# Performance work log

Hardware: AMD Instinct MI355X
Metric: run time of the kernel (lower is better)

## Reference

```python
import jax, jax.numpy as jnp
import numpy as np

N = 50000
E = 800000
IN_CH = 64
HID = 32
HEADS = 8
OUT_CH = 32
NEG_SLOPE = 0.2  # PyG GATConv default leaky_relu slope


def gat_conv(x, src, dst, W, a_src, a_dst, bias, heads, out_ch, concat, n_nodes):
    # x: [N, F_in]; W: [F_in, heads*out_ch]; a_*: [heads, out_ch]; bias: [heads*out_ch] or [out_ch]
    h = (x @ W).reshape(n_nodes, heads, out_ch)            # [N, H, C]
    alpha_s = jnp.sum(h * a_src, axis=-1)                  # [N, H]
    alpha_d = jnp.sum(h * a_dst, axis=-1)                  # [N, H]
    e = jax.nn.leaky_relu(alpha_s[src] + alpha_d[dst], NEG_SLOPE)  # [E, H]
    # segment softmax over destination node
    m = jax.ops.segment_max(e, dst, num_segments=n_nodes)  # [N, H]
    ex = jnp.exp(e - m[dst])                               # [E, H]
    denom = jax.ops.segment_sum(ex, dst, num_segments=n_nodes)  # [N, H]
    alpha = ex / (denom[dst] + 1e-16)                      # [E, H]
    out = jax.ops.segment_sum(alpha[:, :, None] * h[src], dst, num_segments=n_nodes)  # [N, H, C]
    out = out.reshape(n_nodes, heads * out_ch) if concat else out.mean(axis=1)
    return out + bias


def setup_inputs() -> dict:
    key = jax.random.key(0)
    ks = jax.random.split(key, 12)
    x = jax.random.normal(ks[0], (N, IN_CH), dtype=jnp.float32)
    edge_index = jax.random.randint(ks[1], (2, E), 0, N, dtype=jnp.int32)
    s1 = 1.0 / np.sqrt(IN_CH)
    s2 = 1.0 / np.sqrt(HEADS * HID)
    W1 = jax.random.uniform(ks[2], (IN_CH, HEADS * HID), jnp.float32, -s1, s1)
    a_src1 = jax.random.uniform(ks[3], (HEADS, HID), jnp.float32, -s2, s2)
    a_dst1 = jax.random.uniform(ks[4], (HEADS, HID), jnp.float32, -s2, s2)
    b1 = jnp.zeros((HEADS * HID,), jnp.float32)
    W2 = jax.random.uniform(ks[5], (HEADS * HID, OUT_CH), jnp.float32, -s2, s2)
    a_src2 = jax.random.uniform(ks[6], (1, OUT_CH), jnp.float32, -s2, s2)
    a_dst2 = jax.random.uniform(ks[7], (1, OUT_CH), jnp.float32, -s2, s2)
    b2 = jnp.zeros((OUT_CH,), jnp.float32)
    return {"x": x, "edge_index": edge_index, "W1": W1, "a_src1": a_src1,
            "a_dst1": a_dst1, "b1": b1, "W2": W2, "a_src2": a_src2,
            "a_dst2": a_dst2, "b2": b2}


def reference(x, edge_index, W1, a_src1, a_dst1, b1, W2, a_src2, a_dst2, b2):
    # add self-loops (PyG GATConv default)
    loops = jnp.arange(N, dtype=edge_index.dtype)
    src = jnp.concatenate([edge_index[0], loops])
    dst = jnp.concatenate([edge_index[1], loops])
    h = gat_conv(x, src, dst, W1, a_src1, a_dst1, b1, HEADS, HID, True, N)
    h = jax.nn.relu(h)  # dropout inactive in eval
    out = gat_conv(h, src, dst, W2, a_src2, a_dst2, b2, 1, OUT_CH, False, N)
    return jax.nn.log_softmax(out, axis=1)
```

## Files before the change

### kernel.cpp

```cpp
#include <hip/hip_runtime.h>
#include <math.h>
#include <stdint.h>

#define NN 50000
#define NE 800000
#define INC 64
#define HEADS 8
#define F1 256
#define OC 32
#define NEGS 0.2f
#define CSTR 64
#define G1B 1564

typedef unsigned short ushort_t;
typedef float floatx2 __attribute__((ext_vector_type(2)));

__device__ __forceinline__ ushort_t f2bf(float f) {
    uint32_t u = __builtin_bit_cast(uint32_t, f);
    uint32_t r = (u + 0x7fffu + ((u >> 16) & 1u)) >> 16;
    return (ushort_t)r;
}
__device__ __forceinline__ float bflo(uint32_t p) { return __builtin_bit_cast(float, p << 16); }
__device__ __forceinline__ float bfhi(uint32_t p) { return __builtin_bit_cast(float, p & 0xffff0000u); }
__device__ __forceinline__ float bf2f(ushort_t v) { return __builtin_bit_cast(float, (uint32_t)v << 16); }

#if __has_builtin(__builtin_amdgcn_cvt_pk_fp8_f32) && __has_builtin(__builtin_amdgcn_cvt_pk_f32_fp8)
#define HW_FP8 1
#endif

__device__ __forceinline__ uint32_t f2e4m3_sw(float x) {
    float a = fabsf(x);
    uint32_t s = (__builtin_bit_cast(uint32_t, x) >> 31) << 7;
    if (a < 0.015625f) {
        uint32_t m = (uint32_t)rintf(a * 512.0f);
        return s | m;
    }
    if (a >= 448.f) return s | 0x7e;
    uint32_t u = __builtin_bit_cast(uint32_t, a);
    int E = (int)((u >> 23) & 255) - 127;
    float scale = __builtin_bit_cast(float, (uint32_t)(3 - E + 127) << 23);
    uint32_t q = (uint32_t)rintf(a * scale);
    if (q == 16) { E += 1; q = 8; }
    return s | ((uint32_t)(E + 7) << 3) | (q - 8);
}
__device__ __forceinline__ float e4m3f_sw(uint32_t b) {
    uint32_t e = (b >> 3) & 15, m = b & 7;
    float v;
    if (e) v = __builtin_bit_cast(float, ((e + 120u) << 23) | (m << 20));
    else   v = (float)m * 0.001953125f;
    return (b & 0x80u) ? -v : v;
}

__device__ __forceinline__ uint32_t pack4_fp8(float a, float b, float c, float d) {
#ifdef HW_FP8
    int v = __builtin_amdgcn_cvt_pk_fp8_f32(a, b, 0, false);
    v = __builtin_amdgcn_cvt_pk_fp8_f32(c, d, v, true);
    return (uint32_t)v;
#else
    return f2e4m3_sw(a) | (f2e4m3_sw(b) << 8) | (f2e4m3_sw(c) << 16) | (f2e4m3_sw(d) << 24);
#endif
}
__device__ __forceinline__ void unpack4_fp8(uint32_t r, float& f0, float& f1, float& f2, float& f3) {
#ifdef HW_FP8
    floatx2 lo = __builtin_amdgcn_cvt_pk_f32_fp8((int)r, false);
    floatx2 hi = __builtin_amdgcn_cvt_pk_f32_fp8((int)r, true);
    f0 = lo[0]; f1 = lo[1]; f2 = hi[0]; f3 = hi[1];
#else
    f0 = e4m3f_sw(r & 255); f1 = e4m3f_sw((r >> 8) & 255);
    f2 = e4m3f_sw((r >> 16) & 255); f3 = e4m3f_sw(r >> 24);
#endif
}

__global__ __launch_bounds__(256) void k_gemm1(
    const float* __restrict__ x, const float* __restrict__ W1,
    const float* __restrict__ a_s, const float* __restrict__ a_d,
    uint8_t* __restrict__ h1, float* __restrict__ alpha_s, float* __restrict__ alpha_d,
    const int* __restrict__ ei, int* __restrict__ pos, ushort_t* __restrict__ csr_src)
{
    __shared__ float Wl[INC][128];
    __shared__ float xt[INC][64];
    int t = threadIdx.x;
    int gb = blockIdx.x;
    int ntile = gb >> 1;
    int hc = gb & 1;
    int nb = ntile * 64;

    {
        const float* Wsrc = W1 + hc * 128;
        for (int i = t; i < 2048; i += 256) {
            int k = i >> 5, c4 = (i & 31) << 2;
            *(float4*)&Wl[k][c4] = *(const float4*)(Wsrc + k * F1 + c4);
        }
    }
    {
        int n = t >> 2;
        int kq = (t & 3) << 4;
        int gn = nb + n;
        if (gn < NN) {
            const float* xr = x + (size_t)gn * INC + kq;
#pragma unroll
            for (int j = 0; j < 16; j += 4) {
                float4 v = *(const float4*)(xr + j);
                xt[kq + j + 0][n] = v.x; xt[kq + j + 1][n] = v.y;
                xt[kq + j + 2][n] = v.z; xt[kq + j + 3][n] = v.w;
            }
        } else {
#pragma unroll
            for (int j = 0; j < 16; ++j) xt[kq + j][n] = 0.f;
        }
    }
    __syncthreads();

    int lane = t & 63, w = t >> 6;
    int ng = lane >> 5;
    int c0 = (lane & 31) << 2;
    int nbase = (w << 4) + (ng << 3);

    float acc[8][4];
#pragma unroll
    for (int i = 0; i < 8; i++) { acc[i][0] = acc[i][1] = acc[i][2] = acc[i][3] = 0.f; }

#pragma unroll 2
    for (int k = 0; k < INC; ++k) {
        float4 wv = *(const float4*)&Wl[k][c0];
        const float4* xs = (const float4*)&xt[k][nbase];
        float4 xa = xs[0], xb = xs[1];
        float xq[8];
        xq[0] = xa.x; xq[1] = xa.y; xq[2] = xa.z; xq[3] = xa.w;
        xq[4] = xb.x; xq[5] = xb.y; xq[6] = xb.z; xq[7] = xb.w;
#pragma unroll
        for (int ns = 0; ns < 8; ++ns) {
            float xvv = xq[ns];
            acc[ns][0] = fmaf(xvv, wv.x, acc[ns][0]);
            acc[ns][1] = fmaf(xvv, wv.y, acc[ns][1]);
            acc[ns][2] = fmaf(xvv, wv.z, acc[ns][2]);
            acc[ns][3] = fmaf(xvv, wv.w, acc[ns][3]);
        }
    }

    int cglob = hc * 128 + c0;
    float4 av = *(const float4*)(a_s + cglob);
    float4 dv = *(const float4*)(a_d + cglob);
    int head = hc * 4 + ((lane & 31) >> 3);
#pragma unroll
    for (int ns = 0; ns < 8; ++ns) {
        int n = nb + nbase + ns;
        if (n < NN) {
            uint32_t pk = pack4_fp8(acc[ns][0], acc[ns][1], acc[ns][2], acc[ns][3]);
            *(uint32_t*)(h1 + (size_t)n * F1 + cglob) = pk;
            float ps = acc[ns][0] * av.x + acc[ns][1] * av.y + acc[ns][2] * av.z + acc[ns][3] * av.w;
            float pd = acc[ns][0] * dv.x + acc[ns][1] * dv.y + acc[ns][2] * dv.z + acc[ns][3] * dv.w;
            ps += __shfl_xor(ps, 1); ps += __shfl_xor(ps, 2); ps += __shfl_xor(ps, 4);
            pd += __shfl_xor(pd, 1); pd += __shfl_xor(pd, 2); pd += __shfl_xor(pd, 4);
            if ((lane & 7) == 0) {
                alpha_s[n * HEADS + head] = ps;
                alpha_d[n * HEADS + head] = pd;
            }
        }
    }

    {
        int e0 = gb * 512 + t;
#pragma unroll
        for (int q = 0; q < 2; ++q) {
            int e = e0 + q * 256;
            if (e < NE) {
                int s = ei[e];
                int d = ei[NE + e];
                int r = atomicAdd(&pos[d], 1);
                if (r < CSTR) csr_src[d * CSTR + r] = (ushort_t)s;
            }
        }
    }
}

__global__ __launch_bounds__(256) void k_gather1(
    const uint8_t* __restrict__ h1,
    const float* __restrict__ alpha_s, const float* __restrict__ alpha_d,
    const int* __restrict__ pos, const ushort_t* __restrict__ csr_src,
    const float* __restrict__ b1, ushort_t* __restrict__ h1rb)
{
    int wid = (blockIdx.x * blockDim.x + threadIdx.x) >> 6;
    if (wid >= NN) return;
    int lane = threadIdx.x & 63;
    int d = wid;
    int deg = pos[d]; deg = (deg < CSTR) ? deg : CSTR;
    const ushort_t* lst = csr_src + d * CSTR;
    int hh = lane >> 3;
    float ad = alpha_d[d * HEADS + hh];
    int cb = lane << 2;
    const uint8_t* hbase = h1 + cb;

    float4 A0 = {0.f, 0.f, 0.f, 0.f}, A1 = {0.f, 0.f, 0.f, 0.f};
    float dn0 = 0.f, dn1 = 0.f;

    {
        float e = alpha_s[d * HEADS + hh] + ad;
        uint32_t r = *(const uint32_t*)(hbase + (size_t)d * F1);
        e = (e > 0.f) ? e : NEGS * e;
        float w = __expf(e);
        float f0, f1, f2, f3;
        unpack4_fp8(r, f0, f1, f2, f3);
        dn0 += w;
        A0.x = fmaf(w, f0, A0.x); A0.y = fmaf(w, f1, A0.y);
        A0.z = fmaf(w, f2, A0.z); A0.w = fmaf(w, f3, A0.w);
    }

    int i = 0;
    for (; i + 8 <= deg; i += 8) {
        uint4 p4 = *(const uint4*)(lst + i);
        int s[8];
        s[0] = p4.x & 0xffff; s[1] = p4.x >> 16;
        s[2] = p4.y & 0xffff; s[3] = p4.y >> 16;
        s[4] = p4.z & 0xffff; s[5] = p4.z >> 16;
        s[6] = p4.w & 0xffff; s[7] = p4.w >> 16;
        float e[8];
#pragma unroll
        for (int j = 0; j < 8; ++j) e[j] = alpha_s[s[j] * HEADS + hh] + ad;
        uint32_t r[8];
#pragma unroll
        for (int j = 0; j < 8; ++j) r[j] = *(const uint32_t*)(hbase + (size_t)s[j] * F1);
#pragma unroll
        for (int j = 0; j < 8; ++j) {
            float tt = e[j];
            tt = (tt > 0.f) ? tt : NEGS * tt;
            float w = __expf(tt);
            float f0, f1, f2, f3;
            unpack4_fp8(r[j], f0, f1, f2, f3);
            if (j & 1) {
                dn1 += w;
                A1.x = fmaf(w, f0, A1.x); A1.y = fmaf(w, f1, A1.y);
                A1.z = fmaf(w, f2, A1.z); A1.w = fmaf(w, f3, A1.w);
            } else {
                dn0 += w;
                A0.x = fmaf(w, f0, A0.x); A0.y = fmaf(w, f1, A0.y);
                A0.z = fmaf(w, f2, A0.z); A0.w = fmaf(w, f3, A0.w);
            }
        }
    }
    for (; i + 4 <= deg; i += 4) {
        uint2 p2 = *(const uint2*)(lst + i);
        int s0 = p2.x & 0xffff, s1 = p2.x >> 16, s2 = p2.y & 0xffff, s3 = p2.y >> 16;
        float e0 = alpha_s[s0 * HEADS + hh] + ad;
        float e1 = alpha_s[s1 * HEADS + hh] + ad;
        float e2 = alpha_s[s2 * HEADS + hh] + ad;
        float e3 = alpha_s[s3 * HEADS + hh] + ad;
        uint32_t r0 = *(const uint32_t*)(hbase + (size_t)s0 * F1);
        uint32_t r1 = *(const uint32_t*)(hbase + (size_t)s1 * F1);
        uint32_t r2 = *(const uint32_t*)(hbase + (size_t)s2 * F1);
        uint32_t r3 = *(const uint32_t*)(hbase + (size_t)s3 * F1);
        e0 = (e0 > 0.f) ? e0 : NEGS * e0;
        e1 = (e1 > 0.f) ? e1 : NEGS * e1;
        e2 = (e2 > 0.f) ? e2 : NEGS * e2;
        e3 = (e3 > 0.f) ? e3 : NEGS * e3;
        float w0 = __expf(e0), w1 = __expf(e1), w2 = __expf(e2), w3 = __expf(e3);
        float f0, f1, f2, f3;
        dn0 += w0; dn1 += w1; dn0 += w2; dn1 += w3;
        unpack4_fp8(r0, f0, f1, f2, f3);
        A0.x = fmaf(w0, f0, A0.x); A0.y = fmaf(w0, f1, A0.y);
        A0.z = fmaf(w0, f2, A0.z); A0.w = fmaf(w0, f3, A0.w);
        unpack4_fp8(r1, f0, f1, f2, f3);
        A1.x = fmaf(w1, f0, A1.x); A1.y = fmaf(w1, f1, A1.y);
        A1.z = fmaf(w1, f2, A1.z); A1.w = fmaf(w1, f3, A1.w);
        unpack4_fp8(r2, f0, f1, f2, f3);
        A0.x = fmaf(w2, f0, A0.x); A0.y = fmaf(w2, f1, A0.y);
        A0.z = fmaf(w2, f2, A0.z); A0.w = fmaf(w2, f3, A0.w);
        unpack4_fp8(r3, f0, f1, f2, f3);
        A1.x = fmaf(w3, f0, A1.x); A1.y = fmaf(w3, f1, A1.y);
        A1.z = fmaf(w3, f2, A1.z); A1.w = fmaf(w3, f3, A1.w);
    }
    for (; i < deg; ++i) {
        int s = lst[i];
        float e = alpha_s[s * HEADS + hh] + ad;
        uint32_t r = *(const uint32_t*)(hbase + (size_t)s * F1);
        e = (e > 0.f) ? e : NEGS * e;
        float w = __expf(e);
        float f0, f1, f2, f3;
        unpack4_fp8(r, f0, f1, f2, f3);
        dn0 += w;
        A0.x = fmaf(w, f0, A0.x); A0.y = fmaf(w, f1, A0.y);
        A0.z = fmaf(w, f2, A0.z); A0.w = fmaf(w, f3, A0.w);
    }
    float inv = 1.0f / (dn0 + dn1 + 1e-16f);
    float4 bv = *(const float4*)(b1 + cb);
    ushort4 o;
    o.x = f2bf(fmaxf(fmaf(A0.x + A1.x, inv, bv.x), 0.f));
    o.y = f2bf(fmaxf(fmaf(A0.y + A1.y, inv, bv.y), 0.f));
    o.z = f2bf(fmaxf(fmaf(A0.z + A1.z, inv, bv.z), 0.f));
    o.w = f2bf(fmaxf(fmaf(A0.w + A1.w, inv, bv.w), 0.f));
    *(ushort4*)(h1rb + (size_t)d * F1 + cb) = o;
}

#define G2N 256
#define G2K 16
__global__ __launch_bounds__(256) void k_gemm2(
    const ushort_t* __restrict__ h1rb, const float* __restrict__ W2,
    const float* __restrict__ a_s2, const float* __restrict__ a_d2,
    ushort_t* __restrict__ h2b, float* __restrict__ as2o, float* __restrict__ ad2o)
{
    __shared__ float Wl[F1][OC];
    __shared__ float xt[G2K][G2N];
    int t = threadIdx.x;
    for (int i = t; i < F1 * OC / 4; i += 256)
        ((float4*)Wl)[i] = ((const float4*)W2)[i];
    int nb = blockIdx.x * G2N;
    int lane = t & 63, w = t >> 6;
    int g = lane >> 3, c0 = (lane & 7) << 2;

    float acc[8][4];
#pragma unroll
    for (int i = 0; i < 8; i++) { acc[i][0] = acc[i][1] = acc[i][2] = acc[i][3] = 0.f; }

    for (int kc = 0; kc < F1; kc += G2K) {
        __syncthreads();
        {
            int gn = nb + t;
            if (gn < NN) {
                const ushort_t* src = h1rb + (size_t)gn * F1 + kc;
                uint4 v0 = *(const uint4*)src;
                uint4 v1 = *(const uint4*)(src + 8);
                xt[0][t] = bflo(v0.x); xt[1][t] = bfhi(v0.x);
                xt[2][t] = bflo(v0.y); xt[3][t] = bfhi(v0.y);
                xt[4][t] = bflo(v0.z); xt[5][t] = bfhi(v0.z);
                xt[6][t] = bflo(v0.w); xt[7][t] = bfhi(v0.w);
                xt[8][t] = bflo(v1.x); xt[9][t] = bfhi(v1.x);
                xt[10][t] = bflo(v1.y); xt[11][t] = bfhi(v1.y);
                xt[12][t] = bflo(v1.z); xt[13][t] = bfhi(v1.z);
                xt[14][t] = bflo(v1.w); xt[15][t] = bfhi(v1.w);
            } else {
#pragma unroll
                for (int kk = 0; kk < G2K; ++kk) xt[kk][t] = 0.f;
            }
        }
        __syncthreads();
        int nbase = (w << 6) + (g << 3);
#pragma unroll
        for (int kk = 0; kk < G2K; ++kk) {
            float4 wv = *(const float4*)&Wl[kc + kk][c0];
            const float4* xs = (const float4*)&xt[kk][nbase];
            float4 xa = xs[0], xb = xs[1];
            float xq[8];
            xq[0] = xa.x; xq[1] = xa.y; xq[2] = xa.z; xq[3] = xa.w;
            xq[4] = xb.x; xq[5] = xb.y; xq[6] = xb.z; xq[7] = xb.w;
#pragma unroll
            for (int ns = 0; ns < 8; ++ns) {
                float xvv = xq[ns];
                acc[ns][0] = fmaf(xvv, wv.x, acc[ns][0]);
                acc[ns][1] = fmaf(xvv, wv.y, acc[ns][1]);
                acc[ns][2] = fmaf(xvv, wv.z, acc[ns][2]);
                acc[ns][3] = fmaf(xvv, wv.w, acc[ns][3]);
            }
        }
    }

    float4 av = *(const float4*)(a_s2 + c0);
    float4 dv = *(const float4*)(a_d2 + c0);
    int nbase2 = nb + (w << 6) + (g << 3);
#pragma unroll
    for (int ns = 0; ns < 8; ++ns) {
        int n = nbase2 + ns;
        if (n < NN) {
            ushort4 pk;
            pk.x = f2bf(acc[ns][0]); pk.y = f2bf(acc[ns][1]);
            pk.z = f2bf(acc[ns][2]); pk.w = f2bf(acc[ns][3]);
            *(ushort4*)(h2b + (size_t)n * OC + c0) = pk;
            float ps = acc[ns][0] * av.x + acc[ns][1] * av.y + acc[ns][2] * av.z + acc[ns][3] * av.w;
            float pd = acc[ns][0] * dv.x + acc[ns][1] * dv.y + acc[ns][2] * dv.z + acc[ns][3] * dv.w;
            ps += __shfl_xor(ps, 1); ps += __shfl_xor(ps, 2); ps += __shfl_xor(ps, 4);
            pd += __shfl_xor(pd, 1); pd += __shfl_xor(pd, 2); pd += __shfl_xor(pd, 4);
            if ((lane & 7) == 0) { as2o[n] = ps; ad2o[n] = pd; }
        }
    }
}

__global__ __launch_bounds__(256) void k_gather2(
    const ushort_t* __restrict__ h2b,
    const float* __restrict__ as2, const float* __restrict__ ad2,
    const int* __restrict__ pos, const ushort_t* __restrict__ csr_src,
    const float* __restrict__ b2, float* __restrict__ out)
{
    int wid = (blockIdx.x * blockDim.x + threadIdx.x) >> 6;
    if (wid >= NN) return;
    int lane = threadIdx.x & 63;
    int d = wid;
    int deg = pos[d]; deg = (deg < CSTR) ? deg : CSTR;
    const ushort_t* lst = csr_src + d * CSTR;
    int c = lane & 31, half = lane >> 5;
    float ad = ad2[d];
    float accA = 0.f, accB = 0.f, dnA = 0.f, dnB = 0.f;

    if (half == 0) {
        float e = as2[d] + ad;
        float hv = bf2f(h2b[(size_t)d * OC + c]);
        e = (e > 0.f) ? e : NEGS * e;
        float w = __expf(e);
        dnA += w;
        accA = fmaf(w, hv, accA);
    }

    int i = half;
    for (; i + 2 < deg; i += 4) {
        int sA = lst[i];
        int sB = lst[i + 2];
        float eA = as2[sA] + ad;
        float eB = as2[sB] + ad;
        float hA = bf2f(h2b[(size_t)sA * OC + c]);
        float hB = bf2f(h2b[(size_t)sB * OC + c]);
        eA = (eA > 0.f) ? eA : NEGS * eA;
        eB = (eB > 0.f) ? eB : NEGS * eB;
        float wA = __expf(eA), wB = __expf(eB);
        dnA += wA; dnB += wB;
        accA = fmaf(wA, hA, accA); accB = fmaf(wB, hB, accB);
    }
    for (; i < deg; i += 2) {
        int s = lst[i];
        float e = as2[s] + ad;
        float hv = bf2f(h2b[(size_t)s * OC + c]);
        e = (e > 0.f) ? e : NEGS * e;
        float w = __expf(e);
        dnA += w;
        accA = fmaf(w, hv, accA);
    }
    float acc = accA + accB, denom = dnA + dnB;
    acc += __shfl_xor(acc, 32);
    denom += __shfl_xor(denom, 32);
    float v = acc / (denom + 1e-16f) + b2[c];
    float m = v;
#pragma unroll
    for (int mm = 1; mm < 32; mm <<= 1) m = fmaxf(m, __shfl_xor(m, mm));
    float ex = __expf(v - m);
    float se = ex;
#pragma unroll
    for (int mm = 1; mm < 32; mm <<= 1) se += __shfl_xor(se, mm);
    float res = v - m - __logf(se);
    if (half == 0) out[(size_t)d * OC + c] = res;
}


extern "C" void kernel_launch(void* const* d_in, const int* in_sizes, int n_in,
                              void* d_out, int out_size, void* d_ws, size_t ws_size,
                              hipStream_t stream) {
    const float* x   = (const float*)d_in[0];
    const int*   ei  = (const int*)d_in[1];
    const float* W1  = (const float*)d_in[2];
    const float* as1 = (const float*)d_in[3];
    const float* ad1 = (const float*)d_in[4];
    const float* b1  = (const float*)d_in[5];
    const float* W2  = (const float*)d_in[6];
    const float* as2 = (const float*)d_in[7];
    const float* ad2 = (const float*)d_in[8];
    const float* b2  = (const float*)d_in[9];
    float* out = (float*)d_out;

    char* p = (char*)d_ws;
    uint8_t*  h1   = (uint8_t*)p;  p += (size_t)NN * F1;
    ushort_t* h1rb = (ushort_t*)p; p += (size_t)NN * F1 * 2;
    ushort_t* h2b  = (ushort_t*)p; p += (size_t)NN * OC * 2;
    float* a_s1 = (float*)p; p += (size_t)NN * HEADS * 4;
    float* a_d1 = (float*)p; p += (size_t)NN * HEADS * 4;
    float* a_s2 = (float*)p; p += (size_t)NN * 4;
    float* a_d2 = (float*)p; p += (size_t)NN * 4;
    int* pos     = (int*)p; p += (size_t)NN * 4;
    ushort_t* csr_src = (ushort_t*)p; p += (size_t)NN * CSTR * 2;

    hipMemsetAsync(pos, 0, (size_t)NN * 4, stream);

    k_gemm1<<<G1B, 256, 0, stream>>>(x, W1, as1, ad1, h1, a_s1, a_d1, ei, pos, csr_src);

    int gwblocks = (NN + 3) / 4;
    k_gather1<<<gwblocks, 256, 0, stream>>>(h1, a_s1, a_d1, pos, csr_src, b1, h1rb);

    int g2blocks = (NN + G2N - 1) / G2N;
    k_gemm2<<<g2blocks, 256, 0, stream>>>(h1rb, W2, as2, ad2, h2b, a_s2, a_d2);

    k_gather2<<<gwblocks, 256, 0, stream>>>(h2b, a_s2, a_d2, pos, csr_src, b2, out);
}
```

Baseline: 168.0 us.

## Shard destination adjacency buckets across eight counters to cut atomic contention

Splits the per-destination edge bucket into eight shards chosen by the k_gemm1 block index, each with its own counter and 16-slot list, so edge-insertion atomics spread across more addresses. Both gather kernels now merge the shards into a per-wave LDS list, using a lane prefix sum and a serial copy, before the edge loop. This adds merge work and LDS traffic in the gathers, enlarges the counter memset eightfold, and drops edges beyond 16 per shard instead of 64 per node. It also removes the early return for out-of-range waves, and __syncthreads is called after the merge.

New measurement: 179.5 us. 1.07x slower.

```diff
diff --git a/kernel.cpp b/kernel.cpp
--- a/kernel.cpp
+++ b/kernel.cpp
@@ -9,7 +9,8 @@
 #define F1 256
 #define OC 32
 #define NEGS 0.2f
-#define CSTR 64
+#define NSH 8
+#define CSH 16
 #define G1B 1564
 
 typedef unsigned short ushort_t;
@@ -69,6 +70,29 @@
     f0 = e4m3f_sw(r & 255); f1 = e4m3f_sw((r >> 8) & 255);
     f2 = e4m3f_sw((r >> 16) & 255); f3 = e4m3f_sw(r >> 24);
 #endif
+}
+
+__device__ __forceinline__ int merge_shards(
+    const int* __restrict__ pos, const ushort_t* __restrict__ csr,
+    int d, int lane, ushort_t* __restrict__ ml)
+{
+    int degx = 0;
+    if (lane < NSH) {
+        degx = pos[lane * NN + d];
+        degx = (degx < CSH) ? degx : CSH;
+    }
+    int incl = degx;
+#pragma unroll
+    for (int sh = 1; sh < 8; sh <<= 1) {
+        int u = __shfl_up(incl, sh, 8);
+        if ((lane & 7) >= sh) incl += u;
+    }
+    if (lane < NSH) {
+        int off = incl - degx;
+        const ushort_t* row = csr + ((size_t)lane * NN + d) * CSH;
+        for (int j = 0; j < degx; ++j) ml[off + j] = row[j];
+    }
+    return __shfl(incl, 7);
 }
 
 __global__ __launch_bounds__(256) void k_gemm1(
@@ -160,6 +184,9 @@
     }
 
     {
+        int sh = gb & 7;
+        int* shpos = pos + sh * NN;
+        ushort_t* shcsr = csr_src + (size_t)sh * NN * CSH;
         int e0 = gb * 512 + t;
 #pragma unroll
         for (int q = 0; q < 2; ++q) {
@@ -167,8 +194,8 @@
             if (e < NE) {
                 int s = ei[e];
                 int d = ei[NE + e];
-                int r = atomicAdd(&pos[d], 1);
-                if (r < CSTR) csr_src[d * CSTR + r] = (ushort_t)s;
+                int r = atomicAdd(&shpos[d], 1);
+                if (r < CSH) shcsr[(size_t)d * CSH + r] = (ushort_t)s;
             }
         }
     }
@@ -180,12 +207,16 @@
     const int* __restrict__ pos, const ushort_t* __restrict__ csr_src,
     const float* __restrict__ b1, ushort_t* __restrict__ h1rb)
 {
+    __shared__ ushort_t mls[4][NSH * CSH];
+    int wv = threadIdx.x >> 6;
+    int lane = threadIdx.x & 63;
     int wid = (blockIdx.x * blockDim.x + threadIdx.x) >> 6;
-    if (wid >= NN) return;
-    int lane = threadIdx.x & 63;
     int d = wid;
-    int deg = pos[d]; deg = (deg < CSTR) ? deg : CSTR;
-    const ushort_t* lst = csr_src + d * CSTR;
+    ushort_t* ml = mls[wv];
+
+    int total = merge_shards(pos, csr_src, d, lane, ml);
+    __syncthreads();
+
     int hh = lane >> 3;
     float ad = alpha_d[d * HEADS + hh];
     int cb = lane << 2;
@@ -207,8 +238,8 @@
     }
 
     int i = 0;
-    for (; i + 8 <= deg; i += 8) {
-        uint4 p4 = *(const uint4*)(lst + i);
+    for (; i + 8 <= total; i += 8) {
+        uint4 p4 = *(const uint4*)(ml + i);
         int s[8];
         s[0] = p4.x & 0xffff; s[1] = p4.x >> 16;
         s[2] = p4.y & 0xffff; s[3] = p4.y >> 16;
@@ -238,8 +269,8 @@
             }
         }
     }
-    for (; i + 4 <= deg; i += 4) {
-        uint2 p2 = *(const uint2*)(lst + i);
+    for (; i + 4 <= total; i += 4) {
+        uint2 p2 = *(const uint2*)(ml + i);
         int s0 = p2.x & 0xffff, s1 = p2.x >> 16, s2 = p2.y & 0xffff, s3 = p2.y >> 16;
         float e0 = alpha_s[s0 * HEADS + hh] + ad;
         float e1 = alpha_s[s1 * HEADS + hh] + ad;
@@ -269,8 +300,8 @@
         A1.x = fmaf(w3, f0, A1.x); A1.y = fmaf(w3, f1, A1.y);
         A1.z = fmaf(w3, f2, A1.z); A1.w = fmaf(w3, f3, A1.w);
     }
-    for (; i < deg; ++i) {
-        int s = lst[i];
+    for (; i < total; ++i) {
+        int s = ml[i];
         float e = alpha_s[s * HEADS + hh] + ad;
         uint32_t r = *(const uint32_t*)(hbase + (size_t)s * F1);
         e = (e > 0.f) ? e : NEGS * e;
@@ -379,12 +410,16 @@
     const int* __restrict__ pos, const ushort_t* __restrict__ csr_src,
     const float* __restrict__ b2, float* __restrict__ out)
 {
+    __shared__ ushort_t mls[4][NSH * CSH];
+    int wv = threadIdx.x >> 6;
+    int lane = threadIdx.x & 63;
     int wid = (blockIdx.x * blockDim.x + threadIdx.x) >> 6;
-    if (wid >= NN) return;
-    int lane = threadIdx.x & 63;
     int d = wid;
-    int deg = pos[d]; deg = (deg < CSTR) ? deg : CSTR;
-    const ushort_t* lst = csr_src + d * CSTR;
+    ushort_t* ml = mls[wv];
+
+    int total = merge_shards(pos, csr_src, d, lane, ml);
+    __syncthreads();
+
     int c = lane & 31, half = lane >> 5;
     float ad = ad2[d];
     float accA = 0.f, accB = 0.f, dnA = 0.f, dnB = 0.f;
@@ -399,9 +434,9 @@
     }
 
     int i = half;
-    for (; i + 2 < deg; i += 4) {
-        int sA = lst[i];
-        int sB = lst[i + 2];
+    for (; i + 2 < total; i += 4) {
+        int sA = ml[i];
+        int sB = ml[i + 2];
         float eA = as2[sA] + ad;
         float eB = as2[sB] + ad;
         float hA = bf2f(h2b[(size_t)sA * OC + c]);
@@ -412,8 +447,8 @@
         dnA += wA; dnB += wB;
         accA = fmaf(wA, hA, accA); accB = fmaf(wB, hB, accB);
     }
-    for (; i < deg; i += 2) {
-        int s = lst[i];
+    for (; i < total; i += 2) {
+        int s = ml[i];
         float e = as2[s] + ad;
         float hv = bf2f(h2b[(size_t)s * OC + c]);
         e = (e > 0.f) ? e : NEGS * e;
@@ -460,10 +495,10 @@
     float* a_d1 = (float*)p; p += (size_t)NN * HEADS * 4;
     float* a_s2 = (float*)p; p += (size_t)NN * 4;
     float* a_d2 = (float*)p; p += (size_t)NN * 4;
-    int* pos     = (int*)p; p += (size_t)NN * 4;
-    ushort_t* csr_src = (ushort_t*)p; p += (size_t)NN * CSTR * 2;
-
-    hipMemsetAsync(pos, 0, (size_t)NN * 4, stream);
+    int* pos     = (int*)p; p += (size_t)NSH * NN * 4;
+    ushort_t* csr_src = (ushort_t*)p; p += (size_t)NSH * NN * CSH * 2;
+
+    hipMemsetAsync(pos, 0, (size_t)NSH * NN * 4, stream);
 
     k_gemm1<<<G1B, 256, 0, stream>>>(x, W1, as1, ad1, h1, a_s1, a_d1, ei, pos, csr_src);
 
```

## Replace per-node atomic CSR with bucketed edge binning and in-block LDS sort

Applied to the files above, without the earlier changes.

The per-edge global atomic fill of a fixed-stride CSR is replaced by a two-level scheme. Extra blocks in the first GEMM kernel bin edges into 128-node buckets using shared-memory histograms, with one global atomic per bucket per block. Each gather block then counting-sorts its bucket's 32 destination nodes into LDS and processes 8 nodes per wave, reading neighbour ids from LDS. This removes 800K global atomics and scattered 16-bit CSR writes, but each bucket is rescanned by four blocks in both gather kernels. Fixed capacities (BCAP, SENTCAP) can silently drop edges for skewed graphs.

Result: slower. 176.8 us (+5.3%).

```diff
diff --git a/kernel.cpp b/kernel.cpp
--- a/kernel.cpp
+++ b/kernel.cpp
@@ -9,8 +9,12 @@
 #define F1 256
 #define OC 32
 #define NEGS 0.2f
-#define CSTR 64
+
+#define NB 391
+#define BCAP 2432
+#define SCB2 125
 #define G1B 1564
+#define SENTCAP 704
 
 typedef unsigned short ushort_t;
 typedef float floatx2 __attribute__((ext_vector_type(2)));
@@ -75,12 +79,51 @@
     const float* __restrict__ x, const float* __restrict__ W1,
     const float* __restrict__ a_s, const float* __restrict__ a_d,
     uint8_t* __restrict__ h1, float* __restrict__ alpha_s, float* __restrict__ alpha_d,
-    const int* __restrict__ ei, int* __restrict__ pos, ushort_t* __restrict__ csr_src)
+    const int* __restrict__ ei, int* __restrict__ gcnt, uint32_t* __restrict__ gbuf)
 {
-    __shared__ float Wl[INC][128];
-    __shared__ float xt[INC][64];
+    __shared__ __align__(16) char smraw[49152];
+    int b = blockIdx.x;
     int t = threadIdx.x;
-    int gb = blockIdx.x;
+
+    if (b < SCB2) {
+        uint32_t* cnt  = (uint32_t*)smraw;
+        uint32_t* offs = cnt + NB;
+        for (int i = t; i < NB; i += 256) cnt[i] = 0;
+        __syncthreads();
+        const int* dsts = ei + NE;
+        int ebase = b * 6400;
+#pragma unroll
+        for (int j = 0; j < 25; ++j) {
+            int d = dsts[ebase + j * 256 + t];
+            atomicAdd(&cnt[d >> 7], 1u);
+        }
+        __syncthreads();
+        for (int i = t; i < NB; i += 256) {
+            uint32_t c = cnt[i];
+            uint32_t base = 0;
+            if (c) base = (uint32_t)atomicAdd(&gcnt[i], (int)c);
+            if (base > BCAP) base = BCAP;
+            uint32_t end = base + c; if (end > BCAP) end = BCAP;
+            offs[i] = (uint32_t)i * BCAP + base;
+            cnt[i]  = (uint32_t)i * BCAP + end;
+        }
+        __syncthreads();
+#pragma unroll
+        for (int j = 0; j < 25; ++j) {
+            int e = ebase + j * 256 + t;
+            int s = ei[e];
+            int d = dsts[e];
+            int bkt = d >> 7;
+            uint32_t slot = atomicAdd(&offs[bkt], 1u);
+            if (slot < cnt[bkt])
+                gbuf[slot] = ((uint32_t)(d & 127) << 16) | (uint32_t)s;
+        }
+        return;
+    }
+
+    float (*Wl)[128] = (float(*)[128])smraw;
+    float (*xt)[64]  = (float(*)[64])(smraw + 32768);
+    int gb = b - SCB2;
     int ntile = gb >> 1;
     int hc = gb & 1;
     int nb = ntile * 64;
@@ -158,137 +201,174 @@
             }
         }
     }
-
-    {
-        int e0 = gb * 512 + t;
-#pragma unroll
-        for (int q = 0; q < 2; ++q) {
-            int e = e0 + q * 256;
-            if (e < NE) {
-                int s = ei[e];
-                int d = ei[NE + e];
-                int r = atomicAdd(&pos[d], 1);
-                if (r < CSTR) csr_src[d * CSTR + r] = (ushort_t)s;
-            }
-        }
-    }
+}
+
+__device__ __forceinline__ void sort_bucket(
+    const int* __restrict__ gcnt, const uint32_t* __restrict__ gbuf,
+    int sb, int part, int t,
+    uint32_t* __restrict__ scnt, uint32_t* __restrict__ soffs,
+    uint32_t* __restrict__ srun, ushort_t* __restrict__ sent)
+{
+    if (t < 32) scnt[t] = 0;
+    __syncthreads();
+    int cnt = gcnt[sb]; if (cnt > BCAP) cnt = BCAP;
+    const uint32_t* gb_ = gbuf + (size_t)sb * BCAP;
+    int lo = part << 5;
+    for (int i = t; i < cnt; i += 256) {
+        uint32_t v = gb_[i];
+        int dloc = (int)(v >> 16);
+        if ((dloc >> 5) == part) atomicAdd(&scnt[dloc & 31], 1u);
+    }
+    __syncthreads();
+    if (t < 32) {
+        uint32_t c = scnt[t];
+        uint32_t incl = c;
+#pragma unroll
+        for (int sh = 1; sh < 32; sh <<= 1) {
+            uint32_t u = __shfl_up(incl, sh);
+            if (t >= sh) incl += u;
+        }
+        uint32_t off = incl - c;
+        if (off > SENTCAP) off = SENTCAP;
+        soffs[t] = off; srun[t] = off;
+    }
+    __syncthreads();
+    for (int i = t; i < cnt; i += 256) {
+        uint32_t v = gb_[i];
+        int dloc = (int)(v >> 16);
+        if ((dloc >> 5) == part) {
+            uint32_t slot = atomicAdd(&srun[dloc & 31], 1u);
+            if (slot < SENTCAP) sent[slot] = (ushort_t)(v & 0xffffu);
+        }
+    }
+    __syncthreads();
+    (void)lo;
 }
 
 __global__ __launch_bounds__(256) void k_gather1(
     const uint8_t* __restrict__ h1,
     const float* __restrict__ alpha_s, const float* __restrict__ alpha_d,
-    const int* __restrict__ pos, const ushort_t* __restrict__ csr_src,
+    const int* __restrict__ gcnt, const uint32_t* __restrict__ gbuf,
     const float* __restrict__ b1, ushort_t* __restrict__ h1rb)
 {
-    int wid = (blockIdx.x * blockDim.x + threadIdx.x) >> 6;
-    if (wid >= NN) return;
-    int lane = threadIdx.x & 63;
-    int d = wid;
-    int deg = pos[d]; deg = (deg < CSTR) ? deg : CSTR;
-    const ushort_t* lst = csr_src + d * CSTR;
+    __shared__ uint32_t scnt[32], soffs[32], srun[32];
+    __shared__ ushort_t sent[SENTCAP];
+    int t = threadIdx.x;
+    int sb = blockIdx.x >> 2, part = blockIdx.x & 3;
+    int n0 = sb * 128 + part * 32;
+
+    sort_bucket(gcnt, gbuf, sb, part, t, scnt, soffs, srun, sent);
+
+    int lane = t & 63, wv = t >> 6;
     int hh = lane >> 3;
-    float ad = alpha_d[d * HEADS + hh];
     int cb = lane << 2;
     const uint8_t* hbase = h1 + cb;
-
-    float4 A0 = {0.f, 0.f, 0.f, 0.f}, A1 = {0.f, 0.f, 0.f, 0.f};
-    float dn0 = 0.f, dn1 = 0.f;
-
-    {
-        float e = alpha_s[d * HEADS + hh] + ad;
-        uint32_t r = *(const uint32_t*)(hbase + (size_t)d * F1);
-        e = (e > 0.f) ? e : NEGS * e;
-        float w = __expf(e);
-        float f0, f1, f2, f3;
-        unpack4_fp8(r, f0, f1, f2, f3);
-        dn0 += w;
-        A0.x = fmaf(w, f0, A0.x); A0.y = fmaf(w, f1, A0.y);
-        A0.z = fmaf(w, f2, A0.z); A0.w = fmaf(w, f3, A0.w);
-    }
-
-    int i = 0;
-    for (; i + 8 <= deg; i += 8) {
-        uint4 p4 = *(const uint4*)(lst + i);
-        int s[8];
-        s[0] = p4.x & 0xffff; s[1] = p4.x >> 16;
-        s[2] = p4.y & 0xffff; s[3] = p4.y >> 16;
-        s[4] = p4.z & 0xffff; s[5] = p4.z >> 16;
-        s[6] = p4.w & 0xffff; s[7] = p4.w >> 16;
-        float e[8];
-#pragma unroll
-        for (int j = 0; j < 8; ++j) e[j] = alpha_s[s[j] * HEADS + hh] + ad;
-        uint32_t r[8];
-#pragma unroll
-        for (int j = 0; j < 8; ++j) r[j] = *(const uint32_t*)(hbase + (size_t)s[j] * F1);
-#pragma unroll
-        for (int j = 0; j < 8; ++j) {
-            float tt = e[j];
-            tt = (tt > 0.f) ? tt : NEGS * tt;
-            float w = __expf(tt);
+    float4 bv = *(const float4*)(b1 + cb);
+
+    for (int k = 0; k < 8; ++k) {
+        int dloc = wv * 8 + k;
+        int d = n0 + dloc;
+        if (d >= NN) break;
+        int deg = (int)scnt[dloc];
+        uint32_t send = soffs[dloc] + (uint32_t)deg;
+        if (send > SENTCAP) deg = (int)(SENTCAP - soffs[dloc] > 0 ? SENTCAP - soffs[dloc] : 0);
+        const ushort_t* ids = sent + soffs[dloc];
+        float ad = alpha_d[d * HEADS + hh];
+
+        float4 A0 = {0.f, 0.f, 0.f, 0.f}, A1 = {0.f, 0.f, 0.f, 0.f};
+        float dn0 = 0.f, dn1 = 0.f;
+
+        {
+            float e = alpha_s[d * HEADS + hh] + ad;
+            uint32_t r = *(const uint32_t*)(hbase + (size_t)d * F1);
+            e = (e > 0.f) ? e : NEGS * e;
+            float w = __expf(e);
             float f0, f1, f2, f3;
-            unpack4_fp8(r[j], f0, f1, f2, f3);
-            if (j & 1) {
-                dn1 += w;
-                A1.x = fmaf(w, f0, A1.x); A1.y = fmaf(w, f1, A1.y);
-                A1.z = fmaf(w, f2, A1.z); A1.w = fmaf(w, f3, A1.w);
-            } else {
-                dn0 += w;
-                A0.x = fmaf(w, f0, A0.x); A0.y = fmaf(w, f1, A0.y);
-                A0.z = fmaf(w, f2, A0.z); A0.w = fmaf(w, f3, A0.w);
+            unpack4_fp8(r, f0, f1, f2, f3);
+            dn0 += w;
+            A0.x = fmaf(w, f0, A0.x); A0.y = fmaf(w, f1, A0.y);
+            A0.z = fmaf(w, f2, A0.z); A0.w = fmaf(w, f3, A0.w);
+        }
+
+        int i = 0;
+        for (; i + 8 <= deg; i += 8) {
+            int s[8];
+#pragma unroll
+            for (int j = 0; j < 8; ++j) s[j] = ids[i + j];
+            float e[8];
+#pragma unroll
+            for (int j = 0; j < 8; ++j) e[j] = alpha_s[s[j] * HEADS + hh] + ad;
+            uint32_t r[8];
+#pragma unroll
+            for (int j = 0; j < 8; ++j) r[j] = *(const uint32_t*)(hbase + (size_t)s[j] * F1);
+#pragma unroll
+            for (int j = 0; j < 8; ++j) {
+                float tt = e[j];
+                tt = (tt > 0.f) ? tt : NEGS * tt;
+                float w = __expf(tt);
+                float f0, f1, f2, f3;
+                unpack4_fp8(r[j], f0, f1, f2, f3);
+                if (j & 1) {
+                    dn1 += w;
+                    A1.x = fmaf(w, f0, A1.x); A1.y = fmaf(w, f1, A1.y);
+                    A1.z = fmaf(w, f2, A1.z); A1.w = fmaf(w, f3, A1.w);
+                } else {
+                    dn0 += w;
+                    A0.x = fmaf(w, f0, A0.x); A0.y = fmaf(w, f1, A0.y);
+                    A0.z = fmaf(w, f2, A0.z); A0.w = fmaf(w, f3, A0.w);
+                }
             }
         }
-    }
-    for (; i + 4 <= deg; i += 4) {
-        uint2 p2 = *(const uint2*)(lst + i);
-        int s0 = p2.x & 0xffff, s1 = p2.x >> 16, s2 = p2.y & 0xffff, s3 = p2.y >> 16;
-        float e0 = alpha_s[s0 * HEADS + hh] + ad;
-        float e1 = alpha_s[s1 * HEADS + hh] + ad;
-        float e2 = alpha_s[s2 * HEADS + hh] + ad;
-        float e3 = alpha_s[s3 * HEADS + hh] + ad;
-        uint32_t r0 = *(const uint32_t*)(hbase + (size_t)s0 * F1);
-        uint32_t r1 = *(const uint32_t*)(hbase + (size_t)s1 * F1);
-        uint32_t r2 = *(const uint32_t*)(hbase + (size_t)s2 * F1);
-        uint32_t r3 = *(const uint32_t*)(hbase + (size_t)s3 * F1);
-        e0 = (e0 > 0.f) ? e0 : NEGS * e0;
-        e1 = (e1 > 0.f) ? e1 : NEGS * e1;
-        e2 = (e2 > 0.f) ? e2 : NEGS * e2;
-        e3 = (e3 > 0.f) ? e3 : NEGS * e3;
-        float w0 = __expf(e0), w1 = __expf(e1), w2 = __expf(e2), w3 = __expf(e3);
-        float f0, f1, f2, f3;
-        dn0 += w0; dn1 += w1; dn0 += w2; dn1 += w3;
-        unpack4_fp8(r0, f0, f1, f2, f3);
-        A0.x = fmaf(w0, f0, A0.x); A0.y = fmaf(w0, f1, A0.y);
-        A0.z = fmaf(w0, f2, A0.z); A0.w = fmaf(w0, f3, A0.w);
-        unpack4_fp8(r1, f0, f1, f2, f3);
-        A1.x = fmaf(w1, f0, A1.x); A1.y = fmaf(w1, f1, A1.y);
-        A1.z = fmaf(w1, f2, A1.z); A1.w = fmaf(w1, f3, A1.w);
-        unpack4_fp8(r2, f0, f1, f2, f3);
-        A0.x = fmaf(w2, f0, A0.x); A0.y = fmaf(w2, f1, A0.y);
-        A0.z = fmaf(w2, f2, A0.z); A0.w = fmaf(w2, f3, A0.w);
-        unpack4_fp8(r3, f0, f1, f2, f3);
-        A1.x = fmaf(w3, f0, A1.x); A1.y = fmaf(w3, f1, A1.y);
-        A1.z = fmaf(w3, f2, A1.z); A1.w = fmaf(w3, f3, A1.w);
-    }
-    for (; i < deg; ++i) {
-        int s = lst[i];
-        float e = alpha_s[s * HEADS + hh] + ad;
-        uint32_t r = *(const uint32_t*)(hbase + (size_t)s * F1);
-        e = (e > 0.f) ? e : NEGS * e;
-        float w = __expf(e);
-        float f0, f1, f2, f3;
-        unpack4_fp8(r, f0, f1, f2, f3);
-        dn0 += w;
-        A0.x = fmaf(w, f0, A0.x); A0.y = fmaf(w, f1, A0.y);
-        A0.z = fmaf(w, f2, A0.z); A0.w = fmaf(w, f3, A0.w);
-    }
-    float inv = 1.0f / (dn0 + dn1 + 1e-16f);
-    float4 bv = *(const float4*)(b1 + cb);
-    ushort4 o;
-    o.x = f2bf(fmaxf(fmaf(A0.x + A1.x, inv, bv.x), 0.f));
-    o.y = f2bf(fmaxf(fmaf(A0.y + A1.y, inv, bv.y), 0.f));
-    o.z = f2bf(fmaxf(fmaf(A0.z + A1.z, inv, bv.z), 0.f));
-    o.w = f2bf(fmaxf(fmaf(A0.w + A1.w, inv, bv.w), 0.f));
-    *(ushort4*)(h1rb + (size_t)d * F1 + cb) = o;
+        for (; i + 4 <= deg; i += 4) {
+            int s0 = ids[i + 0], s1 = ids[i + 1], s2 = ids[i + 2], s3 = ids[i + 3];
+            float e0 = alpha_s[s0 * HEADS + hh] + ad;
+            float e1 = alpha_s[s1 * HEADS + hh] + ad;
+            float e2 = alpha_s[s2 * HEADS + hh] + ad;
+            float e3 = alpha_s[s3 * HEADS + hh] + ad;
+            uint32_t r0 = *(const uint32_t*)(hbase + (size_t)s0 * F1);
+            uint32_t r1 = *(const uint32_t*)(hbase + (size_t)s1 * F1);
+            uint32_t r2 = *(const uint32_t*)(hbase + (size_t)s2 * F1);
+            uint32_t r3 = *(const uint32_t*)(hbase + (size_t)s3 * F1);
+            e0 = (e0 > 0.f) ? e0 : NEGS * e0;
+            e1 = (e1 > 0.f) ? e1 : NEGS * e1;
+            e2 = (e2 > 0.f) ? e2 : NEGS * e2;
+            e3 = (e3 > 0.f) ? e3 : NEGS * e3;
+            float w0 = __expf(e0), w1 = __expf(e1), w2 = __expf(e2), w3 = __expf(e3);
+            float f0, f1, f2, f3;
+            dn0 += w0; dn1 += w1; dn0 += w2; dn1 += w3;
+            unpack4_fp8(r0, f0, f1, f2, f3);
+            A0.x = fmaf(w0, f0, A0.x); A0.y = fmaf(w0, f1, A0.y);
+            A0.z = fmaf(w0, f2, A0.z); A0.w = fmaf(w0, f3, A0.w);
+            unpack4_fp8(r1, f0, f1, f2, f3);
+            A1.x = fmaf(w1, f0, A1.x); A1.y = fmaf(w1, f1, A1.y);
+            A1.z = fmaf(w1, f2, A1.z); A1.w = fmaf(w1, f3, A1.w);
+            unpack4_fp8(r2, f0, f1, f2, f3);
+            A0.x = fmaf(w2, f0, A0.x); A0.y = fmaf(w2, f1, A0.y);
+            A0.z = fmaf(w2, f2, A0.z); A0.w = fmaf(w2, f3, A0.w);
+            unpack4_fp8(r3, f0, f1, f2, f3);
+            A1.x = fmaf(w3, f0, A1.x); A1.y = fmaf(w3, f1, A1.y);
+            A1.z = fmaf(w3, f2, A1.z); A1.w = fmaf(w3, f3, A1.w);
+        }
+        for (; i < deg; ++i) {
+            int s = ids[i];
+            float e = alpha_s[s * HEADS + hh] + ad;
+            uint32_t r = *(const uint32_t*)(hbase + (size_t)s * F1);
+            e = (e > 0.f) ? e : NEGS * e;
+            float w = __expf(e);
+            float f0, f1, f2, f3;
+            unpack4_fp8(r, f0, f1, f2, f3);
+            dn0 += w;
+            A0.x = fmaf(w, f0, A0.x); A0.y = fmaf(w, f1, A0.y);
+            A0.z = fmaf(w, f2, A0.z); A0.w = fmaf(w, f3, A0.w);
+        }
+        float inv = 1.0f / (dn0 + dn1 + 1e-16f);
+        ushort4 o;
+        o.x = f2bf(fmaxf(fmaf(A0.x + A1.x, inv, bv.x), 0.f));
+        o.y = f2bf(fmaxf(fmaf(A0.y + A1.y, inv, bv.y), 0.f));
+        o.z = f2bf(fmaxf(fmaf(A0.z + A1.z, inv, bv.z), 0.f));
+        o.w = f2bf(fmaxf(fmaf(A0.w + A1.w, inv, bv.w), 0.f));
+        *(ushort4*)(h1rb + (size_t)d * F1 + cb) = o;
+    }
 }
 
 #define G2N 256
@@ -376,64 +456,78 @@
 __global__ __launch_bounds__(256) void k_gather2(
     const ushort_t* __restrict__ h2b,
     const float* __restrict__ as2, const float* __restrict__ ad2,
-    const int* __restrict__ pos, const ushort_t* __restrict__ csr_src,
+    const int* __restrict__ gcnt, const uint32_t* __restrict__ gbuf,
     const float* __restrict__ b2, float* __restrict__ out)
 {
-    int wid = (blockIdx.x * blockDim.x + threadIdx.x) >> 6;
-    if (wid >= NN) return;
-    int lane = threadIdx.x & 63;
-    int d = wid;
-    int deg = pos[d]; deg = (deg < CSTR) ? deg : CSTR;
-    const ushort_t* lst = csr_src + d * CSTR;
+    __shared__ uint32_t scnt[32], soffs[32], srun[32];
+    __shared__ ushort_t sent[SENTCAP];
+    int t = threadIdx.x;
+    int sb = blockIdx.x >> 2, part = blockIdx.x & 3;
+    int n0 = sb * 128 + part * 32;
+
+    sort_bucket(gcnt, gbuf, sb, part, t, scnt, soffs, srun, sent);
+
+    int lane = t & 63, wv = t >> 6;
     int c = lane & 31, half = lane >> 5;
-    float ad = ad2[d];
-    float accA = 0.f, accB = 0.f, dnA = 0.f, dnB = 0.f;
-
-    if (half == 0) {
-        float e = as2[d] + ad;
-        float hv = bf2f(h2b[(size_t)d * OC + c]);
-        e = (e > 0.f) ? e : NEGS * e;
-        float w = __expf(e);
-        dnA += w;
-        accA = fmaf(w, hv, accA);
-    }
-
-    int i = half;
-    for (; i + 2 < deg; i += 4) {
-        int sA = lst[i];
-        int sB = lst[i + 2];
-        float eA = as2[sA] + ad;
-        float eB = as2[sB] + ad;
-        float hA = bf2f(h2b[(size_t)sA * OC + c]);
-        float hB = bf2f(h2b[(size_t)sB * OC + c]);
-        eA = (eA > 0.f) ? eA : NEGS * eA;
-        eB = (eB > 0.f) ? eB : NEGS * eB;
-        float wA = __expf(eA), wB = __expf(eB);
-        dnA += wA; dnB += wB;
-        accA = fmaf(wA, hA, accA); accB = fmaf(wB, hB, accB);
-    }
-    for (; i < deg; i += 2) {
-        int s = lst[i];
-        float e = as2[s] + ad;
-        float hv = bf2f(h2b[(size_t)s * OC + c]);
-        e = (e > 0.f) ? e : NEGS * e;
-        float w = __expf(e);
-        dnA += w;
-        accA = fmaf(w, hv, accA);
-    }
-    float acc = accA + accB, denom = dnA + dnB;
-    acc += __shfl_xor(acc, 32);
-    denom += __shfl_xor(denom, 32);
-    float v = acc / (denom + 1e-16f) + b2[c];
-    float m = v;
-#pragma unroll
-    for (int mm = 1; mm < 32; mm <<= 1) m = fmaxf(m, __shfl_xor(m, mm));
-    float ex = __expf(v - m);
-    float se = ex;
-#pragma unroll
-    for (int mm = 1; mm < 32; mm <<= 1) se += __shfl_xor(se, mm);
-    float res = v - m - __logf(se);
-    if (half == 0) out[(size_t)d * OC + c] = res;
+    float bc = b2[c];
+
+    for (int k = 0; k < 8; ++k) {
+        int dloc = wv * 8 + k;
+        int d = n0 + dloc;
+        if (d >= NN) break;
+        int deg = (int)scnt[dloc];
+        uint32_t send = soffs[dloc] + (uint32_t)deg;
+        if (send > SENTCAP) deg = (int)(SENTCAP - soffs[dloc] > 0 ? SENTCAP - soffs[dloc] : 0);
+        const ushort_t* ids = sent + soffs[dloc];
+        float ad = ad2[d];
+        float accA = 0.f, accB = 0.f, dnA = 0.f, dnB = 0.f;
+
+        if (half == 0) {
+            float e = as2[d] + ad;
+            float hv = bf2f(h2b[(size_t)d * OC + c]);
+            e = (e > 0.f) ? e : NEGS * e;
+            float w = __expf(e);
+            dnA += w;
+            accA = fmaf(w, hv, accA);
+        }
+
+        int i = half;
+        for (; i + 2 < deg; i += 4) {
+            int sA = ids[i];
+            int sB = ids[i + 2];
+            float eA = as2[sA] + ad;
+            float eB = as2[sB] + ad;
+            float hA = bf2f(h2b[(size_t)sA * OC + c]);
+            float hB = bf2f(h2b[(size_t)sB * OC + c]);
+            eA = (eA > 0.f) ? eA : NEGS * eA;
+            eB = (eB > 0.f) ? eB : NEGS * eB;
+            float wA = __expf(eA), wB = __expf(eB);
+            dnA += wA; dnB += wB;
+            accA = fmaf(wA, hA, accA); accB = fmaf(wB, hB, accB);
+        }
+        for (; i < deg; i += 2) {
+            int s = ids[i];
+            float e = as2[s] + ad;
+            float hv = bf2f(h2b[(size_t)s * OC + c]);
+            e = (e > 0.f) ? e : NEGS * e;
+            float w = __expf(e);
+            dnA += w;
+            accA = fmaf(w, hv, accA);
+        }
+        float acc = accA + accB, denom = dnA + dnB;
+        acc += __shfl_xor(acc, 32);
+        denom += __shfl_xor(denom, 32);
+        float v = acc / (denom + 1e-16f) + bc;
+        float m = v;
+#pragma unroll
+        for (int mm = 1; mm < 32; mm <<= 1) m = fmaxf(m, __shfl_xor(m, mm));
+        float ex = __expf(v - m);
+        float se = ex;
+#pragma unroll
+        for (int mm = 1; mm < 32; mm <<= 1) se += __shfl_xor(se, mm);
+        float res = v - m - __logf(se);
+        if (half == 0) out[(size_t)d * OC + c] = res;
+    }
 }
 
 
@@ -460,18 +554,19 @@
     float* a_d1 = (float*)p; p += (size_t)NN * HEADS * 4;
     float* a_s2 = (float*)p; p += (size_t)NN * 4;
     float* a_d2 = (float*)p; p += (size_t)NN * 4;
-    int* pos     = (int*)p; p += (size_t)NN * 4;
-    ushort_t* csr_src = (ushort_t*)p; p += (size_t)NN * CSTR * 2;
-
-    hipMemsetAsync(pos, 0, (size_t)NN * 4, stream);
-
-    k_gemm1<<<G1B, 256, 0, stream>>>(x, W1, as1, ad1, h1, a_s1, a_d1, ei, pos, csr_src);
-
-    int gwblocks = (NN + 3) / 4;
-    k_gather1<<<gwblocks, 256, 0, stream>>>(h1, a_s1, a_d1, pos, csr_src, b1, h1rb);
+    int* gcnt = (int*)p; p += (size_t)((NB + 7) & ~7) * 4;
+    uint32_t* gbuf = (uint32_t*)p; p += (size_t)NB * BCAP * 4;
+
+    hipMemsetAsync(gcnt, 0, (size_t)NB * 4, stream);
+
+    k_gemm1<<<SCB2 + G1B, 256, 0, stream>>>(x, W1, as1, ad1, h1, a_s1, a_d1,
+                                            ei, gcnt, gbuf);
+
+    int gwblocks = NB * 4;
+    k_gather1<<<gwblocks, 256, 0, stream>>>(h1, a_s1, a_d1, gcnt, gbuf, b1, h1rb);
 
     int g2blocks = (NN + G2N - 1) / G2N;
     k_gemm2<<<g2blocks, 256, 0, stream>>>(h1rb, W2, as2, ad2, h2b, a_s2, a_d2);
 
-    k_gather2<<<gwblocks, 256, 0, stream>>>(h2b, a_s2, a_d2, pos, csr_src, b2, out);
-}
+    k_gather2<<<gwblocks, 256, 0, stream>>>(h2b, a_s2, a_d2, gcnt, gbuf, b2, out);
+}
```

## Build CSR via two-pass bucketed scatter instead of per-edge global atomics

Applied to the files above, without the earlier changes.

The edge-to-CSR construction moves out of the GEMM tail. Dedicated blocks of the first kernel now bin edges into 128-node destination buckets using shared-memory counters, with one global atomic per bucket per block. A new transpose kernel then sorts each bucket by destination in shared memory and writes the padded CSR and degree arrays. The aim is to replace roughly 800k contended global atomics and scattered 2-byte writes with mostly coalesced traffic, at the cost of an extra kernel launch, an intermediate buffer, and bucket-capacity truncation if a bucket overflows.

Result: faster. 156.3 us (-7.0%).

```diff
diff --git a/kernel.cpp b/kernel.cpp
--- a/kernel.cpp
+++ b/kernel.cpp
@@ -9,8 +9,12 @@
 #define F1 256
 #define OC 32
 #define NEGS 0.2f
+
+#define NB 391
+#define BCAP 2432
+#define SCB2 125
+#define G1B 1564
 #define CSTR 64
-#define G1B 1564
 
 typedef unsigned short ushort_t;
 typedef float floatx2 __attribute__((ext_vector_type(2)));
@@ -75,12 +79,51 @@
     const float* __restrict__ x, const float* __restrict__ W1,
     const float* __restrict__ a_s, const float* __restrict__ a_d,
     uint8_t* __restrict__ h1, float* __restrict__ alpha_s, float* __restrict__ alpha_d,
-    const int* __restrict__ ei, int* __restrict__ pos, ushort_t* __restrict__ csr_src)
+    const int* __restrict__ ei, int* __restrict__ gcnt, uint32_t* __restrict__ gbuf)
 {
-    __shared__ float Wl[INC][128];
-    __shared__ float xt[INC][64];
+    __shared__ __align__(16) char smraw[49152];
+    int b = blockIdx.x;
     int t = threadIdx.x;
-    int gb = blockIdx.x;
+
+    if (b < SCB2) {
+        uint32_t* cnt  = (uint32_t*)smraw;
+        uint32_t* offs = cnt + NB;
+        for (int i = t; i < NB; i += 256) cnt[i] = 0;
+        __syncthreads();
+        const int* dsts = ei + NE;
+        int ebase = b * 6400;
+#pragma unroll
+        for (int j = 0; j < 25; ++j) {
+            int d = dsts[ebase + j * 256 + t];
+            atomicAdd(&cnt[d >> 7], 1u);
+        }
+        __syncthreads();
+        for (int i = t; i < NB; i += 256) {
+            uint32_t c = cnt[i];
+            uint32_t base = 0;
+            if (c) base = (uint32_t)atomicAdd(&gcnt[i], (int)c);
+            if (base > BCAP) base = BCAP;
+            uint32_t end = base + c; if (end > BCAP) end = BCAP;
+            offs[i] = (uint32_t)i * BCAP + base;
+            cnt[i]  = (uint32_t)i * BCAP + end;
+        }
+        __syncthreads();
+#pragma unroll
+        for (int j = 0; j < 25; ++j) {
+            int e = ebase + j * 256 + t;
+            int s = ei[e];
+            int d = dsts[e];
+            int bkt = d >> 7;
+            uint32_t slot = atomicAdd(&offs[bkt], 1u);
+            if (slot < cnt[bkt])
+                gbuf[slot] = ((uint32_t)(d & 127) << 16) | (uint32_t)s;
+        }
+        return;
+    }
+
+    float (*Wl)[128] = (float(*)[128])smraw;
+    float (*xt)[64]  = (float(*)[64])(smraw + 32768);
+    int gb = b - SCB2;
     int ntile = gb >> 1;
     int hc = gb & 1;
     int nb = ntile * 64;
@@ -158,34 +201,65 @@
             }
         }
     }
-
-    {
-        int e0 = gb * 512 + t;
-#pragma unroll
-        for (int q = 0; q < 2; ++q) {
-            int e = e0 + q * 256;
-            if (e < NE) {
-                int s = ei[e];
-                int d = ei[NE + e];
-                int r = atomicAdd(&pos[d], 1);
-                if (r < CSTR) csr_src[d * CSTR + r] = (ushort_t)s;
-            }
-        }
-    }
+}
+
+__global__ __launch_bounds__(256) void k_transpose(
+    const int* __restrict__ gcnt, const uint32_t* __restrict__ gbuf,
+    ushort_t* __restrict__ csr, int* __restrict__ deg)
+{
+    __shared__ uint32_t cnt[128], off[128], run[128], sc[128];
+    __shared__ ushort_t sent[BCAP];
+    int sb = blockIdx.x;
+    int t = threadIdx.x;
+    if (t < 128) cnt[t] = 0;
+    __syncthreads();
+    int total = gcnt[sb]; if (total > BCAP) total = BCAP;
+    const uint32_t* gb_ = gbuf + (size_t)sb * BCAP;
+
+    for (int i = t; i < total; i += 256) {
+        uint32_t v = gb_[i];
+        atomicAdd(&cnt[v >> 16], 1u);
+    }
+    __syncthreads();
+    if (t < 128) sc[t] = cnt[t];
+    __syncthreads();
+    for (int ofs = 1; ofs < 128; ofs <<= 1) {
+        uint32_t v = 0;
+        if (t < 128 && t >= (uint32_t)ofs) v = sc[t - ofs];
+        __syncthreads();
+        if (t < 128) sc[t] += v;
+        __syncthreads();
+    }
+    if (t < 128) { off[t] = sc[t] - cnt[t]; run[t] = sc[t] - cnt[t]; }
+    __syncthreads();
+    for (int i = t; i < total; i += 256) {
+        uint32_t v = gb_[i];
+        uint32_t slot = atomicAdd(&run[v >> 16], 1u);
+        sent[slot] = (ushort_t)(v & 0xffffu);
+    }
+    __syncthreads();
+    int n = t >> 1, half = t & 1;
+    int dg = (int)cnt[n];
+    if (dg > CSTR) dg = CSTR;
+    int d = sb * 128 + n;
+    if (half == 0) deg[d] = dg;
+    const ushort_t* src = sent + off[n];
+    ushort_t* dst = csr + (size_t)d * CSTR;
+    for (int j = half; j < dg; j += 2) dst[j] = src[j];
 }
 
 __global__ __launch_bounds__(256) void k_gather1(
     const uint8_t* __restrict__ h1,
     const float* __restrict__ alpha_s, const float* __restrict__ alpha_d,
-    const int* __restrict__ pos, const ushort_t* __restrict__ csr_src,
+    const int* __restrict__ deg_, const ushort_t* __restrict__ csr,
     const float* __restrict__ b1, ushort_t* __restrict__ h1rb)
 {
     int wid = (blockIdx.x * blockDim.x + threadIdx.x) >> 6;
     if (wid >= NN) return;
     int lane = threadIdx.x & 63;
     int d = wid;
-    int deg = pos[d]; deg = (deg < CSTR) ? deg : CSTR;
-    const ushort_t* lst = csr_src + d * CSTR;
+    int deg = deg_[d];
+    const ushort_t* lst = csr + (size_t)d * CSTR;
     int hh = lane >> 3;
     float ad = alpha_d[d * HEADS + hh];
     int cb = lane << 2;
@@ -376,15 +450,15 @@
 __global__ __launch_bounds__(256) void k_gather2(
     const ushort_t* __restrict__ h2b,
     const float* __restrict__ as2, const float* __restrict__ ad2,
-    const int* __restrict__ pos, const ushort_t* __restrict__ csr_src,
+    const int* __restrict__ deg_, const ushort_t* __restrict__ csr,
     const float* __restrict__ b2, float* __restrict__ out)
 {
     int wid = (blockIdx.x * blockDim.x + threadIdx.x) >> 6;
     if (wid >= NN) return;
     int lane = threadIdx.x & 63;
     int d = wid;
-    int deg = pos[d]; deg = (deg < CSTR) ? deg : CSTR;
-    const ushort_t* lst = csr_src + d * CSTR;
+    int deg = deg_[d];
+    const ushort_t* lst = csr + (size_t)d * CSTR;
     int c = lane & 31, half = lane >> 5;
     float ad = ad2[d];
     float accA = 0.f, accB = 0.f, dnA = 0.f, dnB = 0.f;
@@ -460,18 +534,23 @@
     float* a_d1 = (float*)p; p += (size_t)NN * HEADS * 4;
     float* a_s2 = (float*)p; p += (size_t)NN * 4;
     float* a_d2 = (float*)p; p += (size_t)NN * 4;
-    int* pos     = (int*)p; p += (size_t)NN * 4;
-    ushort_t* csr_src = (ushort_t*)p; p += (size_t)NN * CSTR * 2;
-
-    hipMemsetAsync(pos, 0, (size_t)NN * 4, stream);
-
-    k_gemm1<<<G1B, 256, 0, stream>>>(x, W1, as1, ad1, h1, a_s1, a_d1, ei, pos, csr_src);
+    int* gcnt = (int*)p; p += (size_t)((NB + 7) & ~7) * 4;
+    uint32_t* gbuf = (uint32_t*)p; p += (size_t)NB * BCAP * 4;
+    ushort_t* csr = (ushort_t*)p; p += (size_t)(NB * 128) * CSTR * 2;
+    int* deg = (int*)p; p += (size_t)(NB * 128) * 4;
+
+    hipMemsetAsync(gcnt, 0, (size_t)NB * 4, stream);
+
+    k_gemm1<<<SCB2 + G1B, 256, 0, stream>>>(x, W1, as1, ad1, h1, a_s1, a_d1,
+                                            ei, gcnt, gbuf);
+
+    k_transpose<<<NB, 256, 0, stream>>>(gcnt, gbuf, csr, deg);
 
     int gwblocks = (NN + 3) / 4;
-    k_gather1<<<gwblocks, 256, 0, stream>>>(h1, a_s1, a_d1, pos, csr_src, b1, h1rb);
+    k_gather1<<<gwblocks, 256, 0, stream>>>(h1, a_s1, a_d1, deg, csr, b1, h1rb);
 
     int g2blocks = (NN + G2N - 1) / G2N;
     k_gemm2<<<g2blocks, 256, 0, stream>>>(h1rb, W2, as2, ad2, h2b, a_s2, a_d2);
 
-    k_gather2<<<gwblocks, 256, 0, stream>>>(h2b, a_s2, a_d2, pos, csr_src, b2, out);
-}
+    k_gather2<<<gwblocks, 256, 0, stream>>>(h2b, a_s2, a_d2, deg, csr, b2, out);
+}
```
